# Kernel tuning notes

Measured on AMD Instinct MI355X. Metric: run time of the kernel, lower is better.

The kernel has to match this reference:

```python
import jax, jax.numpy as jnp
import numpy as np

B, D_IN, D_H, D_F = 65536, 256, 1024, 512


def _linear_init(key, fan_in, fan_out):
    # torch.nn.Linear default: U(-1/sqrt(fan_in), 1/sqrt(fan_in))
    bound = 1.0 / np.sqrt(fan_in)
    kw, kb = jax.random.split(key)
    W = jax.random.uniform(kw, (fan_in, fan_out), minval=-bound, maxval=bound, dtype=jnp.float32)
    b = jax.random.uniform(kb, (fan_out,), minval=-bound, maxval=bound, dtype=jnp.float32)
    return W, b


def setup_inputs() -> dict:
    key = jax.random.key(0)
    ks = jax.random.split(key, 8)
    obs = jax.random.normal(ks[0], (B, D_IN), dtype=jnp.float32)
    # columns 2:4 must be one-hot: [1,0] -> expert b, [0,1] -> expert c
    tag = jax.random.randint(ks[1], (B,), 0, 2).astype(jnp.float32)
    onehot = jnp.stack([tag, 1.0 - tag], axis=1)  # [B, 2]
    obs = obs.at[:, 2:4].set(onehot)
    inp = {"obs": obs}
    for i, name in enumerate(("b", "c", "p")):
        k1, k2 = jax.random.split(ks[2 + i])
        W1, b1 = _linear_init(k1, D_IN, D_H)
        W2, b2 = _linear_init(k2, D_H, D_F)
        inp[f"W1_{name}"] = W1
        inp[f"b1_{name}"] = b1
        inp[f"W2_{name}"] = W2
        inp[f"b2_{name}"] = b2
    return inp


def _mlp(x, W1, b1, W2, b2):
    # Linear -> ReLU -> Linear (tianshou-style MLP, flatten_input=False)
    return jax.nn.relu(x @ W1 + b1) @ W2 + b2


def reference(obs, W1_b, b1_b, W2_b, b2_b, W1_c, b1_c, W2_c, b2_c, W1_p, b1_p, W2_p, b2_p):
    # Vectorized form of the per-row Python loop: compute both experts and the
    # shared branch on the full batch, then select per row by the one-hot tag.
    out_b = _mlp(obs, W1_b, b1_b, W2_b, b2_b)  # [B, D_F]
    out_c = _mlp(obs, W1_c, b1_c, W2_c, b2_c)  # [B, D_F]
    out_p = _mlp(obs, W1_p, b1_p, W2_p, b2_p)  # [B, D_F]
    is_b = (obs[:, 2:3] == 1.0) & (obs[:, 3:4] == 0.0)  # [B, 1]
    expert = jnp.where(is_b, out_b, out_c)
    return jnp.concatenate([expert, out_p], axis=-1)  # [B, 2*D_F]
```

## Files before the change

### kernel.cpp

```cpp
#include <hip/hip_runtime.h>
#include <hip/hip_bf16.h>

#define DIN 256
#define DH  1024
#define DF  512
#define NROWS 65536

#define WS_WTS   0
#define WS_PB    4718592
#define WS_PC    4980736
#define WS_CNT   5242880
#define WS_OFFS  5243904

typedef __attribute__((ext_vector_type(8))) short bf16x8;
typedef __attribute__((ext_vector_type(4))) float f32x4;

__device__ __forceinline__ unsigned short f2b(float f) {
    union { float f; unsigned u; } v; v.f = f;
    unsigned r = v.u + 0x7FFFu + ((v.u >> 16) & 1u);
    return (unsigned short)(r >> 16);
}

__device__ __forceinline__ void gll16(const void* g, void* l) {
    __builtin_amdgcn_global_load_lds(
        (const __attribute__((address_space(1))) void*)g,
        (__attribute__((address_space(3))) void*)l, 16, 0, 0);
}

#define BAR_V(N) asm volatile("s_waitcnt vmcnt(" #N ") lgkmcnt(0)\ns_barrier" ::: "memory")
#define DRAIN_VM() asm volatile("s_waitcnt vmcnt(0)" ::: "memory")

__global__ __launch_bounds__(256) void transpose_to_bf16(
        const float* __restrict__ src, unsigned short* __restrict__ dst,
        int K, int N) {
    __shared__ float tile[64][65];
    int k0 = blockIdx.x * 64, n0 = blockIdx.y * 64;
    int t = threadIdx.x;
    for (int i = 0; i < 16; ++i) {
        int idx = t + i * 256;
        int kk = idx >> 6, nn = idx & 63;
        tile[kk][nn] = src[(size_t)(k0 + kk) * N + (n0 + nn)];
    }
    __syncthreads();
    for (int i = 0; i < 16; ++i) {
        int idx = t + i * 256;
        int nn = idx >> 6, kk = idx & 63;
        dst[(size_t)(n0 + nn) * K + (k0 + kk)] = f2b(tile[kk][nn]);
    }
}

__device__ __forceinline__ int row_tag(const float* obs, int row) {
    float c2 = obs[(size_t)row * DIN + 2];
    float c3 = obs[(size_t)row * DIN + 3];
    return (c2 == 1.0f && c3 == 0.0f) ? 1 : 0;
}

__global__ __launch_bounds__(256) void tag_count(const float* __restrict__ obs,
                                                 int* __restrict__ cnt) {
    int t = threadIdx.x;
    int tag = row_tag(obs, blockIdx.x * 256 + t);
    unsigned long long m = __ballot(tag);
    __shared__ int wc[4];
    if ((t & 63) == 0) wc[t >> 6] = __popcll(m);
    __syncthreads();
    if (t == 0) cnt[blockIdx.x] = wc[0] + wc[1] + wc[2] + wc[3];
}

__global__ __launch_bounds__(256) void scan256(const int* __restrict__ cnt,
                                               int* __restrict__ offs) {
    __shared__ int s[256];
    int t = threadIdx.x;
    s[t] = cnt[t];
    __syncthreads();
    for (int d = 1; d < 256; d <<= 1) {
        int v = (t >= d) ? s[t - d] : 0;
        __syncthreads();
        s[t] += v;
        __syncthreads();
    }
    offs[t] = s[t] - cnt[t];
    if (t == 255) offs[256] = s[255];
}

__global__ __launch_bounds__(256) void fill_perm(const float* __restrict__ obs,
                                                 const int* __restrict__ offs,
                                                 int* __restrict__ pb,
                                                 int* __restrict__ pc) {
    int t = threadIdx.x, bid = blockIdx.x;
    int row = bid * 256 + t;
    int tag = row_tag(obs, row);
    unsigned long long m = __ballot(tag);
    __shared__ int wc[4];
    int lane = t & 63, wv = t >> 6;
    if (lane == 0) wc[wv] = __popcll(m);
    __syncthreads();
    int woff = 0;
    for (int i = 0; i < 4; ++i) if (i < wv) woff += wc[i];
    int lb = woff + __popcll(m & ((1ull << lane) - 1ull));
    int base_b = offs[bid];
    if (tag) pb[base_b + lb] = row;
    else     pc[bid * 256 - base_b + (t - lb)] = row;
}

__global__ __launch_bounds__(512, 2) void fused_mlp(
    const float* __restrict__ obs,
    const unsigned short* __restrict__ wts,
    const int* __restrict__ perm_b, const int* __restrict__ perm_c,
    const int* __restrict__ offs,
    const float* __restrict__ b1_0, const float* __restrict__ b2_0,
    const float* __restrict__ b1_1, const float* __restrict__ b2_1,
    const float* __restrict__ b1_2, const float* __restrict__ b2_2,
    float* __restrict__ out)
{
    extern __shared__ char lds[];
    char* ldsX  = lds;
    char* ldsW1 = lds + 65536;
    char* ldsQA = lds + 98304;
    char* ldsQB = lds + 114688;
    char* ldsH  = lds + 131072;
    float* ldsB1 = (float*)(lds + 147456);
    float* ldsB2 = (float*)(lds + 151552);
    int*  ldsPr  = (int*)(lds + 153600);

    const int ob = blockIdx.x;
    const int xcd = ob & 7, ii = ob >> 3;
    const int bid = (xcd == 0) ? ii : (129 + (xcd - 1) * 128 + ii);

    int branch, base, cnt;
    const int* perm;
    if (bid < 512) {
        branch = 2; base = bid * 128; cnt = NROWS; perm = nullptr;
    } else {
        int eb = bid - 512;
        int nb = offs[256];
        int nbb = (nb + 127) >> 7;
        int nc = NROWS - nb;
        int ncb = (nc + 127) >> 7;
        if (eb < nbb)            { branch = 0; base = eb * 128;         cnt = nb; perm = perm_b; }
        else if (eb < nbb + ncb) { branch = 1; base = (eb - nbb) * 128; cnt = nc; perm = perm_c; }
        else return;
    }

    const float* b1 = branch == 0 ? b1_0 : (branch == 1 ? b1_1 : b1_2);
    const float* b2 = branch == 0 ? b2_0 : (branch == 1 ? b2_1 : b2_2);
    const char* w1t = (const char*)(wts + (size_t)branch * (DH * DIN));
    const char* w2t = (const char*)(wts + (size_t)3 * DH * DIN + (size_t)branch * (DF * DH));

    const int t = threadIdx.x;
    const int lane = t & 63;
    const int w = t >> 6;
    const int l15 = lane & 15;
    const int g = lane >> 4;

    ldsB1[t] = b1[t];
    ldsB1[t + 512] = b1[t + 512];
    ldsB2[t] = b2[t];
    if (t < 128) {
        int gr = base + t;
        ldsPr[t] = (gr < cnt) ? (perm ? perm[gr] : gr) : -1;
    }
    #pragma unroll
    for (int i = 0; i < 16; ++i) {
        int idx = t + i * 512;
        int r = idx >> 6, c4 = idx & 63;
        int gr = base + r;
        int grow = gr < cnt ? gr : cnt - 1;
        if (perm) grow = perm[grow];
        f32x4 v = *(const f32x4*)(obs + (size_t)grow * DIN + c4 * 4);
        ushort4 p4;
        p4.x = f2b(v.x); p4.y = f2b(v.y); p4.z = f2b(v.z); p4.w = f2b(v.w);
        *(ushort4*)(ldsX + r * 512 + ((c4 * 8) ^ ((r & 7) << 4))) = p4;
    }
    DRAIN_VM();

    #define STAGE_Q(buf, q, hc_)                                               \
        {                                                                      \
            _Pragma("unroll")                                                  \
            for (int i = 0; i < 2; ++i) {                                      \
                int slot = t + i * 512;                                        \
                int nl = slot >> 3, boff = (slot & 7) << 4;                    \
                gll16(w2t + (size_t)((q) * 128 + nl) * 2048 + (hc_) * 128      \
                          + (boff ^ ((nl & 7) << 4)),                          \
                      (buf) + slot * 16);                                      \
            }                                                                  \
        }

    #define STAGE_W1(hc_)                                                      \
        {                                                                      \
            _Pragma("unroll")                                                  \
            for (int i = 0; i < 4; ++i) {                                      \
                int slot = t + i * 512;                                        \
                int nl = slot >> 5, boff = (slot & 31) << 4;                   \
                gll16(w1t + (size_t)((hc_) * 64 + nl) * 512 + (boff ^ ((nl & 7) << 4)), \
                      ldsW1 + slot * 16);                                      \
            }                                                                  \
        }

    STAGE_W1(0);
    STAGE_Q(ldsQA, 0, 0);
    BAR_V(2);

    const int rg = w & 3, cg = w >> 2;
    const int wr = w >> 2, wc = w & 3;

    const int ar0 = rg * 32 + l15, ar1 = ar0 + 16;
    const int asw0 = (ar0 & 7) << 4, asw1 = (ar1 & 7) << 4;
    const int bn0 = cg * 32 + l15, bn1 = bn0 + 16;
    const int bsw0 = (bn0 & 7) << 4, bsw1 = (bn1 & 7) << 4;

    f32x4 acc[4][8];
    #pragma unroll
    for (int a = 0; a < 4; ++a)
        #pragma unroll
        for (int b = 0; b < 8; ++b)
            #pragma unroll
            for (int e = 0; e < 4; ++e) acc[a][b][e] = 0.0f;

    #define QUARTER_MFMA(buf, c0)                                              \
        {                                                                      \
            _Pragma("unroll")                                                  \
            for (int k2 = 0; k2 < 2; ++k2)                                     \
                _Pragma("unroll")                                              \
                for (int ct = 0; ct < 2; ++ct) {                               \
                    int fr = wc * 32 + ct * 16 + l15;                          \
                    bf16x8 bb = *(const bf16x8*)((buf) + fr * 128 +            \
                                 ((k2 * 64 + g * 16) ^ ((fr & 7) << 4)));      \
                    _Pragma("unroll")                                          \
                    for (int rt = 0; rt < 4; ++rt)                             \
                        acc[rt][(c0) + ct] = __builtin_amdgcn_mfma_f32_16x16x32_bf16( \
                            hA[rt][k2], bb, acc[rt][(c0) + ct], 0, 0, 0);      \
                }                                                              \
        }

    for (int hc = 0; hc < 16; ++hc) {
        STAGE_Q(ldsQB, 1, hc);
        f32x4 aH[2][2];
        #pragma unroll
        for (int a = 0; a < 2; ++a)
            #pragma unroll
            for (int b = 0; b < 2; ++b)
                #pragma unroll
                for (int e = 0; e < 4; ++e) aH[a][b][e] = 0.0f;
        __builtin_amdgcn_s_setprio(1);
        #pragma unroll
        for (int kk = 0; kk < 8; ++kk) {
            int kb = kk * 64 + g * 16;
            bf16x8 a0 = *(const bf16x8*)(ldsX  + ar0 * 512 + (kb ^ asw0));
            bf16x8 a1 = *(const bf16x8*)(ldsX  + ar1 * 512 + (kb ^ asw1));
            bf16x8 b0 = *(const bf16x8*)(ldsW1 + bn0 * 512 + (kb ^ bsw0));
            bf16x8 b1f = *(const bf16x8*)(ldsW1 + bn1 * 512 + (kb ^ bsw1));
            aH[0][0] = __builtin_amdgcn_mfma_f32_16x16x32_bf16(a0, b0,  aH[0][0], 0, 0, 0);
            aH[0][1] = __builtin_amdgcn_mfma_f32_16x16x32_bf16(a0, b1f, aH[0][1], 0, 0, 0);
            aH[1][0] = __builtin_amdgcn_mfma_f32_16x16x32_bf16(a1, b0,  aH[1][0], 0, 0, 0);
            aH[1][1] = __builtin_amdgcn_mfma_f32_16x16x32_bf16(a1, b1f, aH[1][1], 0, 0, 0);
        }
        __builtin_amdgcn_s_setprio(0);
        {
            float b1v0 = ldsB1[hc * 64 + cg * 32 + l15];
            float b1v1 = ldsB1[hc * 64 + cg * 32 + 16 + l15];
            #pragma unroll
            for (int art = 0; art < 2; ++art)
                #pragma unroll
                for (int bct = 0; bct < 2; ++bct) {
                    int col2 = (cg * 32 + bct * 16 + l15) * 2;
                    float bv = bct ? b1v1 : b1v0;
                    #pragma unroll
                    for (int r = 0; r < 4; ++r) {
                        int hrow = rg * 32 + art * 16 + g * 4 + r;
                        float vv = fmaxf(aH[art][bct][r] + bv, 0.0f);
                        *(unsigned short*)(ldsH + hrow * 128 + (col2 ^ ((hrow & 7) << 4))) = f2b(vv);
                    }
                }
        }
        BAR_V(2);

        bf16x8 hA[4][2];
        #pragma unroll
        for (int rt = 0; rt < 4; ++rt)
            #pragma unroll
            for (int k2 = 0; k2 < 2; ++k2) {
                int hr = wr * 64 + rt * 16 + l15;
                hA[rt][k2] = *(const bf16x8*)(ldsH + hr * 128 + ((k2 * 64 + g * 16) ^ ((hr & 7) << 4)));
            }
        __builtin_amdgcn_s_setprio(1);
        QUARTER_MFMA(ldsQA, 0);
        __builtin_amdgcn_s_setprio(0);
        BAR_V(0);

        STAGE_Q(ldsQA, 2, hc);
        __builtin_amdgcn_s_setprio(1);
        QUARTER_MFMA(ldsQB, 2);
        __builtin_amdgcn_s_setprio(0);
        BAR_V(0);

        STAGE_Q(ldsQB, 3, hc);
        STAGE_W1((hc + 1) & 15);
        __builtin_amdgcn_s_setprio(1);
        QUARTER_MFMA(ldsQA, 4);
        __builtin_amdgcn_s_setprio(0);
        BAR_V(4);

        STAGE_Q(ldsQA, 0, (hc + 1) & 15);
        __builtin_amdgcn_s_setprio(1);
        QUARTER_MFMA(ldsQB, 6);
        __builtin_amdgcn_s_setprio(0);
        BAR_V(2);
    }
    DRAIN_VM();

    int colq[8]; float b2v[8];
    #pragma unroll
    for (int q = 0; q < 8; ++q) {
        colq[q] = (q >> 1) * 128 + wc * 32 + (q & 1) * 16 + l15;
        b2v[q] = ldsB2[colq[q]];
    }
    const int cb = (branch == 2) ? DF : 0;
    #pragma unroll
    for (int rt = 0; rt < 4; ++rt)
        #pragma unroll
        for (int r = 0; r < 4; ++r) {
            int row = wr * 64 + rt * 16 + g * 4 + r;
            int prow = ldsPr[row];
            if (prow >= 0) {
                float* op = out + (size_t)prow * (2 * DF) + cb;
                #pragma unroll
                for (int q = 0; q < 8; ++q)
                    op[colq[q]] = acc[rt][q][r] + b2v[q];
            }
        }
}

extern "C" void kernel_launch(void* const* d_in, const int* in_sizes, int n_in,
                              void* d_out, int out_size, void* d_ws, size_t ws_size,
                              hipStream_t stream) {
    const float* obs = (const float*)d_in[0];
    const float* W1[3] = {(const float*)d_in[1], (const float*)d_in[5], (const float*)d_in[9]};
    const float* b1[3] = {(const float*)d_in[2], (const float*)d_in[6], (const float*)d_in[10]};
    const float* W2[3] = {(const float*)d_in[3], (const float*)d_in[7], (const float*)d_in[11]};
    const float* b2[3] = {(const float*)d_in[4], (const float*)d_in[8], (const float*)d_in[12]};

    char* ws = (char*)d_ws;
    unsigned short* wts = (unsigned short*)(ws + WS_WTS);
    int* pb   = (int*)(ws + WS_PB);
    int* pc   = (int*)(ws + WS_PC);
    int* cnt  = (int*)(ws + WS_CNT);
    int* offs = (int*)(ws + WS_OFFS);

    for (int br = 0; br < 3; ++br) {
        transpose_to_bf16<<<dim3(DIN / 64, DH / 64), 256, 0, stream>>>(
            W1[br], wts + (size_t)br * DH * DIN, DIN, DH);
        transpose_to_bf16<<<dim3(DH / 64, DF / 64), 256, 0, stream>>>(
            W2[br], wts + (size_t)3 * DH * DIN + (size_t)br * DF * DH, DH, DF);
    }
    tag_count<<<256, 256, 0, stream>>>(obs, cnt);
    scan256<<<1, 256, 0, stream>>>(cnt, offs);
    fill_perm<<<256, 256, 0, stream>>>(obs, offs, pb, pc);

    hipFuncSetAttribute((const void*)fused_mlp,
                        hipFuncAttributeMaxDynamicSharedMemorySize, 154112);
    fused_mlp<<<1025, 512, 154112, stream>>>(obs, wts, pb, pc, offs,
        b1[0], b2[0], b1[1], b2[1], b1[2], b2[2], (float*)d_out);
}
```

Before: 341.8 us.

## Merge expert permutations into one array and handle the boundary tile in two passes

The b and c row permutations are written into a single contiguous array, so the expert tiles cover exactly 512 full 128-row tiles. The one tile that straddles the b/c boundary runs two passes, one per expert weight set, and each pass writes only its own row range. This removes the padded partial tiles and the wasted extra block, cutting the grid from 1025 to 1024 blocks so it divides evenly across CUs. In exchange, one block does twice the work, which may lengthen the tail, and the shared per-block setup now runs inside a pass loop.

```diff
diff --git a/kernel.cpp b/kernel.cpp
--- a/kernel.cpp
+++ b/kernel.cpp
@@ -7,8 +7,7 @@
 #define NROWS 65536
 
 #define WS_WTS   0
-#define WS_PB    4718592
-#define WS_PC    4980736
+#define WS_U     4718592
 #define WS_CNT   5242880
 #define WS_OFFS  5243904
 
@@ -82,10 +81,9 @@
     if (t == 255) offs[256] = s[255];
 }
 
-__global__ __launch_bounds__(256) void fill_perm(const float* __restrict__ obs,
-                                                 const int* __restrict__ offs,
-                                                 int* __restrict__ pb,
-                                                 int* __restrict__ pc) {
+__global__ __launch_bounds__(256) void fill_permU(const float* __restrict__ obs,
+                                                  const int* __restrict__ offs,
+                                                  int* __restrict__ U) {
     int t = threadIdx.x, bid = blockIdx.x;
     int row = bid * 256 + t;
     int tag = row_tag(obs, row);
@@ -98,15 +96,15 @@
     for (int i = 0; i < 4; ++i) if (i < wv) woff += wc[i];
     int lb = woff + __popcll(m & ((1ull << lane) - 1ull));
     int base_b = offs[bid];
-    if (tag) pb[base_b + lb] = row;
-    else     pc[bid * 256 - base_b + (t - lb)] = row;
+    int nb = offs[256];
+    if (tag) U[base_b + lb] = row;
+    else     U[nb + bid * 256 - base_b + (t - lb)] = row;
 }
 
 __global__ __launch_bounds__(512, 2) void fused_mlp(
     const float* __restrict__ obs,
     const unsigned short* __restrict__ wts,
-    const int* __restrict__ perm_b, const int* __restrict__ perm_c,
-    const int* __restrict__ offs,
+    const int* __restrict__ U, const int* __restrict__ offs,
     const float* __restrict__ b1_0, const float* __restrict__ b2_0,
     const float* __restrict__ b1_1, const float* __restrict__ b2_1,
     const float* __restrict__ b1_2, const float* __restrict__ b2_2,
@@ -123,28 +121,30 @@
     int*  ldsPr  = (int*)(lds + 153600);
 
     const int ob = blockIdx.x;
-    const int xcd = ob & 7, ii = ob >> 3;
-    const int bid = (xcd == 0) ? ii : (129 + (xcd - 1) * 128 + ii);
-
-    int branch, base, cnt;
-    const int* perm;
-    if (bid < 512) {
-        branch = 2; base = bid * 128; cnt = NROWS; perm = nullptr;
+    const int wid = (ob & 7) * 128 + (ob >> 3);
+
+    const int nb = offs[256];
+    int e_mix = nb >> 7; if (e_mix > 511) e_mix = 511;
+    const int rb = nb - e_mix * 128;
+
+    int base, npass, brA, loA, hiA;
+    int brB = 1, loB = 0, hiB = 0;
+    bool usePerm;
+    if (wid == 0) {
+        base = e_mix * 128; usePerm = true;
+        if (rb > 0 && rb < 128) { npass = 2; brA = 0; loA = 0; hiA = rb;
+                                  brB = 1; loB = rb; hiB = 128; }
+        else if (rb == 0)       { npass = 1; brA = 1; loA = 0; hiA = 128; }
+        else                    { npass = 1; brA = 0; loA = 0; hiA = 128; }
+    } else if (wid <= 512) {
+        base = (wid - 1) * 128; usePerm = false;
+        npass = 1; brA = 2; loA = 0; hiA = 128;
     } else {
-        int eb = bid - 512;
-        int nb = offs[256];
-        int nbb = (nb + 127) >> 7;
-        int nc = NROWS - nb;
-        int ncb = (nc + 127) >> 7;
-        if (eb < nbb)            { branch = 0; base = eb * 128;         cnt = nb; perm = perm_b; }
-        else if (eb < nbb + ncb) { branch = 1; base = (eb - nbb) * 128; cnt = nc; perm = perm_c; }
-        else return;
-    }
-
-    const float* b1 = branch == 0 ? b1_0 : (branch == 1 ? b1_1 : b1_2);
-    const float* b2 = branch == 0 ? b2_0 : (branch == 1 ? b2_1 : b2_2);
-    const char* w1t = (const char*)(wts + (size_t)branch * (DH * DIN));
-    const char* w2t = (const char*)(wts + (size_t)3 * DH * DIN + (size_t)branch * (DF * DH));
+        int j = wid - 513;
+        int e = (j < e_mix) ? j : j + 1;
+        base = e * 128; usePerm = true;
+        npass = 1; brA = (e < e_mix) ? 0 : 1; loA = 0; hiA = 128;
+    }
 
     const int t = threadIdx.x;
     const int lane = t & 63;
@@ -152,26 +152,25 @@
     const int l15 = lane & 15;
     const int g = lane >> 4;
 
-    ldsB1[t] = b1[t];
-    ldsB1[t + 512] = b1[t + 512];
-    ldsB2[t] = b2[t];
-    if (t < 128) {
-        int gr = base + t;
-        ldsPr[t] = (gr < cnt) ? (perm ? perm[gr] : gr) : -1;
-    }
+    if (t < 128) ldsPr[t] = usePerm ? U[base + t] : (base + t);
     #pragma unroll
     for (int i = 0; i < 16; ++i) {
         int idx = t + i * 512;
         int r = idx >> 6, c4 = idx & 63;
-        int gr = base + r;
-        int grow = gr < cnt ? gr : cnt - 1;
-        if (perm) grow = perm[grow];
+        int grow = usePerm ? U[base + r] : (base + r);
         f32x4 v = *(const f32x4*)(obs + (size_t)grow * DIN + c4 * 4);
         ushort4 p4;
         p4.x = f2b(v.x); p4.y = f2b(v.y); p4.z = f2b(v.z); p4.w = f2b(v.w);
         *(ushort4*)(ldsX + r * 512 + ((c4 * 8) ^ ((r & 7) << 4))) = p4;
     }
-    DRAIN_VM();
+
+    const int rg = w & 3, cg = w >> 2;
+    const int wr = w >> 2, wc = w & 3;
+
+    const int ar0 = rg * 32 + l15, ar1 = ar0 + 16;
+    const int asw0 = (ar0 & 7) << 4, asw1 = (ar1 & 7) << 4;
+    const int bn0 = cg * 32 + l15, bn1 = bn0 + 16;
+    const int bsw0 = (bn0 & 7) << 4, bsw1 = (bn1 & 7) << 4;
 
     #define STAGE_Q(buf, q, hc_)                                               \
         {                                                                      \
@@ -195,26 +194,6 @@
                       ldsW1 + slot * 16);                                      \
             }                                                                  \
         }
-
-    STAGE_W1(0);
-    STAGE_Q(ldsQA, 0, 0);
-    BAR_V(2);
-
-    const int rg = w & 3, cg = w >> 2;
-    const int wr = w >> 2, wc = w & 3;
-
-    const int ar0 = rg * 32 + l15, ar1 = ar0 + 16;
-    const int asw0 = (ar0 & 7) << 4, asw1 = (ar1 & 7) << 4;
-    const int bn0 = cg * 32 + l15, bn1 = bn0 + 16;
-    const int bsw0 = (bn0 & 7) << 4, bsw1 = (bn1 & 7) << 4;
-
-    f32x4 acc[4][8];
-    #pragma unroll
-    for (int a = 0; a < 4; ++a)
-        #pragma unroll
-        for (int b = 0; b < 8; ++b)
-            #pragma unroll
-            for (int e = 0; e < 4; ++e) acc[a][b][e] = 0.0f;
 
     #define QUARTER_MFMA(buf, c0)                                              \
         {                                                                      \
@@ -232,102 +211,130 @@
                 }                                                              \
         }
 
-    for (int hc = 0; hc < 16; ++hc) {
-        STAGE_Q(ldsQB, 1, hc);
-        f32x4 aH[2][2];
+    for (int pass = 0; pass < npass; ++pass) {
+        const int branch = (pass == 0) ? brA : brB;
+        const int rlo = (pass == 0) ? loA : loB;
+        const int rhi = (pass == 0) ? hiA : hiB;
+        const float* b1 = branch == 0 ? b1_0 : (branch == 1 ? b1_1 : b1_2);
+        const float* b2 = branch == 0 ? b2_0 : (branch == 1 ? b2_1 : b2_2);
+        const char* w1t = (const char*)(wts + (size_t)branch * (DH * DIN));
+        const char* w2t = (const char*)(wts + (size_t)3 * DH * DIN + (size_t)branch * (DF * DH));
+
+        ldsB1[t] = b1[t];
+        ldsB1[t + 512] = b1[t + 512];
+        ldsB2[t] = b2[t];
+        DRAIN_VM();
+
+        STAGE_W1(0);
+        STAGE_Q(ldsQA, 0, 0);
+        BAR_V(2);
+
+        f32x4 acc[4][8];
         #pragma unroll
-        for (int a = 0; a < 2; ++a)
-            #pragma unroll
-            for (int b = 0; b < 2; ++b)
+        for (int a = 0; a < 4; ++a)
+            #pragma unroll
+            for (int b = 0; b < 8; ++b)
                 #pragma unroll
-                for (int e = 0; e < 4; ++e) aH[a][b][e] = 0.0f;
-        __builtin_amdgcn_s_setprio(1);
+                for (int e = 0; e < 4; ++e) acc[a][b][e] = 0.0f;
+
+        for (int hc = 0; hc < 16; ++hc) {
+            STAGE_Q(ldsQB, 1, hc);
+            f32x4 aH[2][2];
+            #pragma unroll
+            for (int a = 0; a < 2; ++a)
+                #pragma unroll
+                for (int b = 0; b < 2; ++b)
+                    #pragma unroll
+                    for (int e = 0; e < 4; ++e) aH[a][b][e] = 0.0f;
+            __builtin_amdgcn_s_setprio(1);
+            #pragma unroll
+            for (int kk = 0; kk < 8; ++kk) {
+                int kb = kk * 64 + g * 16;
+                bf16x8 a0 = *(const bf16x8*)(ldsX  + ar0 * 512 + (kb ^ asw0));
+                bf16x8 a1 = *(const bf16x8*)(ldsX  + ar1 * 512 + (kb ^ asw1));
+                bf16x8 b0 = *(const bf16x8*)(ldsW1 + bn0 * 512 + (kb ^ bsw0));
+                bf16x8 b1f = *(const bf16x8*)(ldsW1 + bn1 * 512 + (kb ^ bsw1));
+                aH[0][0] = __builtin_amdgcn_mfma_f32_16x16x32_bf16(a0, b0,  aH[0][0], 0, 0, 0);
+                aH[0][1] = __builtin_amdgcn_mfma_f32_16x16x32_bf16(a0, b1f, aH[0][1], 0, 0, 0);
+                aH[1][0] = __builtin_amdgcn_mfma_f32_16x16x32_bf16(a1, b0,  aH[1][0], 0, 0, 0);
+                aH[1][1] = __builtin_amdgcn_mfma_f32_16x16x32_bf16(a1, b1f, aH[1][1], 0, 0, 0);
+            }
+            __builtin_amdgcn_s_setprio(0);
+            {
+                float b1v0 = ldsB1[hc * 64 + cg * 32 + l15];
+                float b1v1 = ldsB1[hc * 64 + cg * 32 + 16 + l15];
+                #pragma unroll
+                for (int art = 0; art < 2; ++art)
+                    #pragma unroll
+                    for (int bct = 0; bct < 2; ++bct) {
+                        int col2 = (cg * 32 + bct * 16 + l15) * 2;
+                        float bv = bct ? b1v1 : b1v0;
+                        #pragma unroll
+                        for (int r = 0; r < 4; ++r) {
+                            int hrow = rg * 32 + art * 16 + g * 4 + r;
+                            float vv = fmaxf(aH[art][bct][r] + bv, 0.0f);
+                            *(unsigned short*)(ldsH + hrow * 128 + (col2 ^ ((hrow & 7) << 4))) = f2b(vv);
+                        }
+                    }
+            }
+            BAR_V(2);
+
+            bf16x8 hA[4][2];
+            #pragma unroll
+            for (int rt = 0; rt < 4; ++rt)
+                #pragma unroll
+                for (int k2 = 0; k2 < 2; ++k2) {
+                    int hr = wr * 64 + rt * 16 + l15;
+                    hA[rt][k2] = *(const bf16x8*)(ldsH + hr * 128 + ((k2 * 64 + g * 16) ^ ((hr & 7) << 4)));
+                }
+            __builtin_amdgcn_s_setprio(1);
+            QUARTER_MFMA(ldsQA, 0);
+            __builtin_amdgcn_s_setprio(0);
+            BAR_V(0);
+
+            STAGE_Q(ldsQA, 2, hc);
+            __builtin_amdgcn_s_setprio(1);
+            QUARTER_MFMA(ldsQB, 2);
+            __builtin_amdgcn_s_setprio(0);
+            BAR_V(0);
+
+            STAGE_Q(ldsQB, 3, hc);
+            STAGE_W1((hc + 1) & 15);
+            __builtin_amdgcn_s_setprio(1);
+            QUARTER_MFMA(ldsQA, 4);
+            __builtin_amdgcn_s_setprio(0);
+            BAR_V(4);
+
+            STAGE_Q(ldsQA, 0, (hc + 1) & 15);
+            __builtin_amdgcn_s_setprio(1);
+            QUARTER_MFMA(ldsQB, 6);
+            __builtin_amdgcn_s_setprio(0);
+            BAR_V(2);
+        }
+        DRAIN_VM();
+
+        const int colbase = (branch == 2) ? DF : 0;
+        int colq[8]; float b2v[8];
         #pragma unroll
-        for (int kk = 0; kk < 8; ++kk) {
-            int kb = kk * 64 + g * 16;
-            bf16x8 a0 = *(const bf16x8*)(ldsX  + ar0 * 512 + (kb ^ asw0));
-            bf16x8 a1 = *(const bf16x8*)(ldsX  + ar1 * 512 + (kb ^ asw1));
-            bf16x8 b0 = *(const bf16x8*)(ldsW1 + bn0 * 512 + (kb ^ bsw0));
-            bf16x8 b1f = *(const bf16x8*)(ldsW1 + bn1 * 512 + (kb ^ bsw1));
-            aH[0][0] = __builtin_amdgcn_mfma_f32_16x16x32_bf16(a0, b0,  aH[0][0], 0, 0, 0);
-            aH[0][1] = __builtin_amdgcn_mfma_f32_16x16x32_bf16(a0, b1f, aH[0][1], 0, 0, 0);
-            aH[1][0] = __builtin_amdgcn_mfma_f32_16x16x32_bf16(a1, b0,  aH[1][0], 0, 0, 0);
-            aH[1][1] = __builtin_amdgcn_mfma_f32_16x16x32_bf16(a1, b1f, aH[1][1], 0, 0, 0);
-        }
-        __builtin_amdgcn_s_setprio(0);
-        {
-            float b1v0 = ldsB1[hc * 64 + cg * 32 + l15];
-            float b1v1 = ldsB1[hc * 64 + cg * 32 + 16 + l15];
-            #pragma unroll
-            for (int art = 0; art < 2; ++art)
-                #pragma unroll
-                for (int bct = 0; bct < 2; ++bct) {
-                    int col2 = (cg * 32 + bct * 16 + l15) * 2;
-                    float bv = bct ? b1v1 : b1v0;
-                    #pragma unroll
-                    for (int r = 0; r < 4; ++r) {
-                        int hrow = rg * 32 + art * 16 + g * 4 + r;
-                        float vv = fmaxf(aH[art][bct][r] + bv, 0.0f);
-                        *(unsigned short*)(ldsH + hrow * 128 + (col2 ^ ((hrow & 7) << 4))) = f2b(vv);
-                    }
-                }
-        }
-        BAR_V(2);
-
-        bf16x8 hA[4][2];
+        for (int q = 0; q < 8; ++q) {
+            colq[q] = (q >> 1) * 128 + wc * 32 + (q & 1) * 16 + l15;
+            b2v[q] = ldsB2[colq[q]];
+        }
         #pragma unroll
         for (int rt = 0; rt < 4; ++rt)
             #pragma unroll
-            for (int k2 = 0; k2 < 2; ++k2) {
-                int hr = wr * 64 + rt * 16 + l15;
-                hA[rt][k2] = *(const bf16x8*)(ldsH + hr * 128 + ((k2 * 64 + g * 16) ^ ((hr & 7) << 4)));
+            for (int r = 0; r < 4; ++r) {
+                int row = wr * 64 + rt * 16 + g * 4 + r;
+                if (row >= rlo && row < rhi) {
+                    int prow = ldsPr[row];
+                    float* op = out + (size_t)prow * (2 * DF) + colbase;
+                    #pragma unroll
+                    for (int q = 0; q < 8; ++q)
+                        op[colq[q]] = acc[rt][q][r] + b2v[q];
+                }
             }
-        __builtin_amdgcn_s_setprio(1);
-        QUARTER_MFMA(ldsQA, 0);
-        __builtin_amdgcn_s_setprio(0);
-        BAR_V(0);
-
-        STAGE_Q(ldsQA, 2, hc);
-        __builtin_amdgcn_s_setprio(1);
-        QUARTER_MFMA(ldsQB, 2);
-        __builtin_amdgcn_s_setprio(0);
-        BAR_V(0);
-
-        STAGE_Q(ldsQB, 3, hc);
-        STAGE_W1((hc + 1) & 15);
-        __builtin_amdgcn_s_setprio(1);
-        QUARTER_MFMA(ldsQA, 4);
-        __builtin_amdgcn_s_setprio(0);
-        BAR_V(4);
-
-        STAGE_Q(ldsQA, 0, (hc + 1) & 15);
-        __builtin_amdgcn_s_setprio(1);
-        QUARTER_MFMA(ldsQB, 6);
-        __builtin_amdgcn_s_setprio(0);
-        BAR_V(2);
-    }
-    DRAIN_VM();
-
-    int colq[8]; float b2v[8];
-    #pragma unroll
-    for (int q = 0; q < 8; ++q) {
-        colq[q] = (q >> 1) * 128 + wc * 32 + (q & 1) * 16 + l15;
-        b2v[q] = ldsB2[colq[q]];
-    }
-    const int cb = (branch == 2) ? DF : 0;
-    #pragma unroll
-    for (int rt = 0; rt < 4; ++rt)
-        #pragma unroll
-        for (int r = 0; r < 4; ++r) {
-            int row = wr * 64 + rt * 16 + g * 4 + r;
-            int prow = ldsPr[row];
-            if (prow >= 0) {
-                float* op = out + (size_t)prow * (2 * DF) + cb;
-                #pragma unroll
-                for (int q = 0; q < 8; ++q)
-                    op[colq[q]] = acc[rt][q][r] + b2v[q];
-            }
-        }
+        __syncthreads();
+    }
 }
 
 extern "C" void kernel_launch(void* const* d_in, const int* in_sizes, int n_in,
@@ -341,8 +348,7 @@
 
     char* ws = (char*)d_ws;
     unsigned short* wts = (unsigned short*)(ws + WS_WTS);
-    int* pb   = (int*)(ws + WS_PB);
-    int* pc   = (int*)(ws + WS_PC);
+    int* U    = (int*)(ws + WS_U);
     int* cnt  = (int*)(ws + WS_CNT);
     int* offs = (int*)(ws + WS_OFFS);
 
@@ -354,10 +360,10 @@
     }
     tag_count<<<256, 256, 0, stream>>>(obs, cnt);
     scan256<<<1, 256, 0, stream>>>(cnt, offs);
-    fill_perm<<<256, 256, 0, stream>>>(obs, offs, pb, pc);
+    fill_permU<<<256, 256, 0, stream>>>(obs, offs, U);
 
     hipFuncSetAttribute((const void*)fused_mlp,
                         hipFuncAttributeMaxDynamicSharedMemorySize, 154112);
-    fused_mlp<<<1025, 512, 154112, stream>>>(obs, wts, pb, pc, offs,
+    fused_mlp<<<1024, 512, 154112, stream>>>(obs, wts, U, offs,
         b1[0], b2[0], b1[1], b2[1], b1[2], b2[2], (float*)d_out);
 }
```

Result: slower. 353.1 us (+3.3%).

## Split last shared-branch tile across two half-width blocks to balance tail

Applied to the files above, without the earlier changes.

Changes block-to-work mapping: the last shared-branch 128-row tile is split into two blocks that each compute half of the output columns (two quarters of W2), launched as blocks 1024 and 1025. The XCD remapping is simplified to a contiguous per-XCD workid scheme. This aims to shorten the tail wave when 1025 full tiles exceed even distribution across CUs, at the cost of recomputing GEMM1 for that tile twice and extra code paths.

```diff
diff --git a/kernel.cpp b/kernel.cpp
--- a/kernel.cpp
+++ b/kernel.cpp
@@ -123,22 +123,25 @@
     int*  ldsPr  = (int*)(lds + 153600);
 
     const int ob = blockIdx.x;
-    const int xcd = ob & 7, ii = ob >> 3;
-    const int bid = (xcd == 0) ? ii : (129 + (xcd - 1) * 128 + ii);
-
-    int branch, base, cnt;
+    int branch, base, cnt, half = -1;
     const int* perm;
-    if (bid < 512) {
-        branch = 2; base = bid * 128; cnt = NROWS; perm = nullptr;
+    if (ob >= 1024) {
+        half = ob - 1024;
+        branch = 2; base = 511 * 128; cnt = NROWS; perm = nullptr;
     } else {
-        int eb = bid - 512;
-        int nb = offs[256];
-        int nbb = (nb + 127) >> 7;
-        int nc = NROWS - nb;
-        int ncb = (nc + 127) >> 7;
-        if (eb < nbb)            { branch = 0; base = eb * 128;         cnt = nb; perm = perm_b; }
-        else if (eb < nbb + ncb) { branch = 1; base = (eb - nbb) * 128; cnt = nc; perm = perm_c; }
-        else return;
+        const int wid = (ob & 7) * 128 + (ob >> 3);
+        if (wid < 511) {
+            branch = 2; base = wid * 128; cnt = NROWS; perm = nullptr;
+        } else {
+            int eb = wid - 511;
+            int nb = offs[256];
+            int nbb = (nb + 127) >> 7;
+            int nc = NROWS - nb;
+            int ncb = (nc + 127) >> 7;
+            if (eb < nbb)            { branch = 0; base = eb * 128;         cnt = nb; perm = perm_b; }
+            else if (eb < nbb + ncb) { branch = 1; base = (eb - nbb) * 128; cnt = nc; perm = perm_c; }
+            else return;
+        }
     }
 
     const float* b1 = branch == 0 ? b1_0 : (branch == 1 ? b1_1 : b1_2);
@@ -196,10 +199,6 @@
             }                                                                  \
         }
 
-    STAGE_W1(0);
-    STAGE_Q(ldsQA, 0, 0);
-    BAR_V(2);
-
     const int rg = w & 3, cg = w >> 2;
     const int wr = w >> 2, wc = w & 3;
 
@@ -215,6 +214,56 @@
         for (int b = 0; b < 8; ++b)
             #pragma unroll
             for (int e = 0; e < 4; ++e) acc[a][b][e] = 0.0f;
+
+    #define GEMM1_BODY(hc_)                                                    \
+        f32x4 aH[2][2];                                                        \
+        _Pragma("unroll")                                                      \
+        for (int a = 0; a < 2; ++a)                                            \
+            _Pragma("unroll")                                                  \
+            for (int b = 0; b < 2; ++b)                                        \
+                _Pragma("unroll")                                              \
+                for (int e = 0; e < 4; ++e) aH[a][b][e] = 0.0f;                \
+        __builtin_amdgcn_s_setprio(1);                                         \
+        _Pragma("unroll")                                                      \
+        for (int kk = 0; kk < 8; ++kk) {                                       \
+            int kb = kk * 64 + g * 16;                                         \
+            bf16x8 a0 = *(const bf16x8*)(ldsX  + ar0 * 512 + (kb ^ asw0));     \
+            bf16x8 a1 = *(const bf16x8*)(ldsX  + ar1 * 512 + (kb ^ asw1));     \
+            bf16x8 b0 = *(const bf16x8*)(ldsW1 + bn0 * 512 + (kb ^ bsw0));     \
+            bf16x8 b1f = *(const bf16x8*)(ldsW1 + bn1 * 512 + (kb ^ bsw1));    \
+            aH[0][0] = __builtin_amdgcn_mfma_f32_16x16x32_bf16(a0, b0,  aH[0][0], 0, 0, 0); \
+            aH[0][1] = __builtin_amdgcn_mfma_f32_16x16x32_bf16(a0, b1f, aH[0][1], 0, 0, 0); \
+            aH[1][0] = __builtin_amdgcn_mfma_f32_16x16x32_bf16(a1, b0,  aH[1][0], 0, 0, 0); \
+            aH[1][1] = __builtin_amdgcn_mfma_f32_16x16x32_bf16(a1, b1f, aH[1][1], 0, 0, 0); \
+        }                                                                      \
+        __builtin_amdgcn_s_setprio(0);                                         \
+        {                                                                      \
+            float b1v0 = ldsB1[(hc_) * 64 + cg * 32 + l15];                    \
+            float b1v1 = ldsB1[(hc_) * 64 + cg * 32 + 16 + l15];               \
+            _Pragma("unroll")                                                  \
+            for (int art = 0; art < 2; ++art)                                  \
+                _Pragma("unroll")                                              \
+                for (int bct = 0; bct < 2; ++bct) {                            \
+                    int col2 = (cg * 32 + bct * 16 + l15) * 2;                 \
+                    float bv = bct ? b1v1 : b1v0;                              \
+                    _Pragma("unroll")                                          \
+                    for (int r = 0; r < 4; ++r) {                              \
+                        int hrow = rg * 32 + art * 16 + g * 4 + r;             \
+                        float vv = fmaxf(aH[art][bct][r] + bv, 0.0f);          \
+                        *(unsigned short*)(ldsH + hrow * 128 + (col2 ^ ((hrow & 7) << 4))) = f2b(vv); \
+                    }                                                          \
+                }                                                              \
+        }
+
+    #define LOAD_HA()                                                          \
+        bf16x8 hA[4][2];                                                       \
+        _Pragma("unroll")                                                      \
+        for (int rt = 0; rt < 4; ++rt)                                         \
+            _Pragma("unroll")                                                  \
+            for (int k2 = 0; k2 < 2; ++k2) {                                   \
+                int hr = wr * 64 + rt * 16 + l15;                              \
+                hA[rt][k2] = *(const bf16x8*)(ldsH + hr * 128 + ((k2 * 64 + g * 16) ^ ((hr & 7) << 4))); \
+            }
 
     #define QUARTER_MFMA(buf, c0)                                              \
         {                                                                      \
@@ -232,102 +281,111 @@
                 }                                                              \
         }
 
-    for (int hc = 0; hc < 16; ++hc) {
-        STAGE_Q(ldsQB, 1, hc);
-        f32x4 aH[2][2];
+    if (half < 0) {
+        STAGE_W1(0);
+        STAGE_Q(ldsQA, 0, 0);
+        BAR_V(2);
+
+        for (int hc = 0; hc < 16; ++hc) {
+            STAGE_Q(ldsQB, 1, hc);
+            GEMM1_BODY(hc);
+            BAR_V(2);
+
+            LOAD_HA();
+            __builtin_amdgcn_s_setprio(1);
+            QUARTER_MFMA(ldsQA, 0);
+            __builtin_amdgcn_s_setprio(0);
+            BAR_V(0);
+
+            STAGE_Q(ldsQA, 2, hc);
+            __builtin_amdgcn_s_setprio(1);
+            QUARTER_MFMA(ldsQB, 2);
+            __builtin_amdgcn_s_setprio(0);
+            BAR_V(0);
+
+            STAGE_Q(ldsQB, 3, hc);
+            STAGE_W1((hc + 1) & 15);
+            __builtin_amdgcn_s_setprio(1);
+            QUARTER_MFMA(ldsQA, 4);
+            __builtin_amdgcn_s_setprio(0);
+            BAR_V(4);
+
+            STAGE_Q(ldsQA, 0, (hc + 1) & 15);
+            __builtin_amdgcn_s_setprio(1);
+            QUARTER_MFMA(ldsQB, 6);
+            __builtin_amdgcn_s_setprio(0);
+            BAR_V(2);
+        }
+        DRAIN_VM();
+
+        int colq[8]; float b2v[8];
         #pragma unroll
-        for (int a = 0; a < 2; ++a)
-            #pragma unroll
-            for (int b = 0; b < 2; ++b)
-                #pragma unroll
-                for (int e = 0; e < 4; ++e) aH[a][b][e] = 0.0f;
-        __builtin_amdgcn_s_setprio(1);
-        #pragma unroll
-        for (int kk = 0; kk < 8; ++kk) {
-            int kb = kk * 64 + g * 16;
-            bf16x8 a0 = *(const bf16x8*)(ldsX  + ar0 * 512 + (kb ^ asw0));
-            bf16x8 a1 = *(const bf16x8*)(ldsX  + ar1 * 512 + (kb ^ asw1));
-            bf16x8 b0 = *(const bf16x8*)(ldsW1 + bn0 * 512 + (kb ^ bsw0));
-            bf16x8 b1f = *(const bf16x8*)(ldsW1 + bn1 * 512 + (kb ^ bsw1));
-            aH[0][0] = __builtin_amdgcn_mfma_f32_16x16x32_bf16(a0, b0,  aH[0][0], 0, 0, 0);
-            aH[0][1] = __builtin_amdgcn_mfma_f32_16x16x32_bf16(a0, b1f, aH[0][1], 0, 0, 0);
-            aH[1][0] = __builtin_amdgcn_mfma_f32_16x16x32_bf16(a1, b0,  aH[1][0], 0, 0, 0);
-            aH[1][1] = __builtin_amdgcn_mfma_f32_16x16x32_bf16(a1, b1f, aH[1][1], 0, 0, 0);
-        }
-        __builtin_amdgcn_s_setprio(0);
-        {
-            float b1v0 = ldsB1[hc * 64 + cg * 32 + l15];
-            float b1v1 = ldsB1[hc * 64 + cg * 32 + 16 + l15];
-            #pragma unroll
-            for (int art = 0; art < 2; ++art)
-                #pragma unroll
-                for (int bct = 0; bct < 2; ++bct) {
-                    int col2 = (cg * 32 + bct * 16 + l15) * 2;
-                    float bv = bct ? b1v1 : b1v0;
-                    #pragma unroll
-                    for (int r = 0; r < 4; ++r) {
-                        int hrow = rg * 32 + art * 16 + g * 4 + r;
-                        float vv = fmaxf(aH[art][bct][r] + bv, 0.0f);
-                        *(unsigned short*)(ldsH + hrow * 128 + (col2 ^ ((hrow & 7) << 4))) = f2b(vv);
-                    }
-                }
-        }
-        BAR_V(2);
-
-        bf16x8 hA[4][2];
+        for (int q = 0; q < 8; ++q) {
+            colq[q] = (q >> 1) * 128 + wc * 32 + (q & 1) * 16 + l15;
+            b2v[q] = ldsB2[colq[q]];
+        }
+        const int cb = (branch == 2) ? DF : 0;
         #pragma unroll
         for (int rt = 0; rt < 4; ++rt)
             #pragma unroll
-            for (int k2 = 0; k2 < 2; ++k2) {
-                int hr = wr * 64 + rt * 16 + l15;
-                hA[rt][k2] = *(const bf16x8*)(ldsH + hr * 128 + ((k2 * 64 + g * 16) ^ ((hr & 7) << 4)));
+            for (int r = 0; r < 4; ++r) {
+                int row = wr * 64 + rt * 16 + g * 4 + r;
+                int prow = ldsPr[row];
+                if (prow >= 0) {
+                    float* op = out + (size_t)prow * (2 * DF) + cb;
+                    #pragma unroll
+                    for (int q = 0; q < 8; ++q)
+                        op[colq[q]] = acc[rt][q][r] + b2v[q];
+                }
             }
-        __builtin_amdgcn_s_setprio(1);
-        QUARTER_MFMA(ldsQA, 0);
-        __builtin_amdgcn_s_setprio(0);
-        BAR_V(0);
-
-        STAGE_Q(ldsQA, 2, hc);
-        __builtin_amdgcn_s_setprio(1);
-        QUARTER_MFMA(ldsQB, 2);
-        __builtin_amdgcn_s_setprio(0);
-        BAR_V(0);
-
-        STAGE_Q(ldsQB, 3, hc);
-        STAGE_W1((hc + 1) & 15);
-        __builtin_amdgcn_s_setprio(1);
-        QUARTER_MFMA(ldsQA, 4);
-        __builtin_amdgcn_s_setprio(0);
-        BAR_V(4);
-
-        STAGE_Q(ldsQA, 0, (hc + 1) & 15);
-        __builtin_amdgcn_s_setprio(1);
-        QUARTER_MFMA(ldsQB, 6);
-        __builtin_amdgcn_s_setprio(0);
+    } else {
+        const int qlo = half * 2, qhi = qlo + 1;
+        STAGE_W1(0);
+        if (half == 0) { STAGE_Q(ldsQA, 0, 0); } else { STAGE_Q(ldsQA, 2, 0); }
         BAR_V(2);
-    }
-    DRAIN_VM();
-
-    int colq[8]; float b2v[8];
-    #pragma unroll
-    for (int q = 0; q < 8; ++q) {
-        colq[q] = (q >> 1) * 128 + wc * 32 + (q & 1) * 16 + l15;
-        b2v[q] = ldsB2[colq[q]];
-    }
-    const int cb = (branch == 2) ? DF : 0;
-    #pragma unroll
-    for (int rt = 0; rt < 4; ++rt)
+
+        for (int hc = 0; hc < 16; ++hc) {
+            if (half == 0) { STAGE_Q(ldsQB, 1, hc); } else { STAGE_Q(ldsQB, 3, hc); }
+            GEMM1_BODY(hc);
+            BAR_V(2);
+
+            LOAD_HA();
+            STAGE_W1((hc + 1) & 15);
+            __builtin_amdgcn_s_setprio(1);
+            QUARTER_MFMA(ldsQA, 0);
+            __builtin_amdgcn_s_setprio(0);
+            BAR_V(4);
+
+            if (half == 0) { STAGE_Q(ldsQA, 0, (hc + 1) & 15); }
+            else           { STAGE_Q(ldsQA, 2, (hc + 1) & 15); }
+            __builtin_amdgcn_s_setprio(1);
+            QUARTER_MFMA(ldsQB, 2);
+            __builtin_amdgcn_s_setprio(0);
+            BAR_V(2);
+        }
+        DRAIN_VM();
+
+        int colq[4]; float b2v[4];
         #pragma unroll
-        for (int r = 0; r < 4; ++r) {
-            int row = wr * 64 + rt * 16 + g * 4 + r;
-            int prow = ldsPr[row];
-            if (prow >= 0) {
-                float* op = out + (size_t)prow * (2 * DF) + cb;
-                #pragma unroll
-                for (int q = 0; q < 8; ++q)
-                    op[colq[q]] = acc[rt][q][r] + b2v[q];
+        for (int q = 0; q < 4; ++q) {
+            colq[q] = (q >> 1) * 128 + wc * 32 + (q & 1) * 16 + l15;
+            b2v[q] = ldsB2[half * 256 + colq[q]];
+        }
+        const int cb = DF + half * 256;
+        #pragma unroll
+        for (int rt = 0; rt < 4; ++rt)
+            #pragma unroll
+            for (int r = 0; r < 4; ++r) {
+                int row = wr * 64 + rt * 16 + g * 4 + r;
+                int prow = ldsPr[row];
+                if (prow >= 0) {
+                    float* op = out + (size_t)prow * (2 * DF) + cb;
+                    #pragma unroll
+                    for (int q = 0; q < 4; ++q)
+                        op[colq[q]] = acc[rt][q][r] + b2v[q];
+                }
             }
-        }
+    }
 }
 
 extern "C" void kernel_launch(void* const* d_in, const int* in_sizes, int n_in,
@@ -358,6 +416,6 @@
 
     hipFuncSetAttribute((const void*)fused_mlp,
                         hipFuncAttributeMaxDynamicSharedMemorySize, 154112);
-    fused_mlp<<<1025, 512, 154112, stream>>>(obs, wts, pb, pc, offs,
+    fused_mlp<<<1026, 512, 154112, stream>>>(obs, wts, pb, pc, offs,
         b1[0], b2[0], b1[1], b2[1], b1[2], b2[2], (float*)d_out);
 }
```

Result: no change. 335.3 us (-1.9%).
